# Kernel optimization log

Hardware: AMD Instinct MI355X
Metric: run time of the kernel (lower is better)

The kernel has to match this reference:

```python
import jax, jax.numpy as jnp
import numpy as np

N_NODES = 100000
T = 1024        # number of visits / hyperedges (GRU sequence length)
IN = 128        # in_channel
HID = 256       # hid_channel


def setup_inputs() -> dict:
    key = jax.random.key(0)
    ks = jax.random.split(key, 7)
    X = jax.random.normal(ks[0], (N_NODES, IN), dtype=jnp.float32)
    H = jax.random.uniform(ks[1], (N_NODES, T), dtype=jnp.float32)
    s = 1.0 / np.sqrt(HID)  # torch default GRU init scale
    w_ih = jax.random.uniform(ks[2], (3 * HID, IN), jnp.float32, -s, s)
    w_hh = jax.random.uniform(ks[3], (3 * HID, HID), jnp.float32, -s, s)
    b_ih = jax.random.uniform(ks[4], (3 * HID,), jnp.float32, -s, s)
    b_hh = jax.random.uniform(ks[5], (3 * HID,), jnp.float32, -s, s)
    w_attn = jax.random.uniform(ks[6], (HID,), jnp.float32, -s, s)
    return {"X": X, "H": H, "w_ih": w_ih, "w_hh": w_hh,
            "b_ih": b_ih, "b_hh": b_hh, "w_attn": w_attn}


def _gru(visit_emb, w_ih, w_hh, b_ih, b_hh):
    # Precompute input-side gates for all timesteps: [T, 3H]
    gx = visit_emb @ w_ih.T + b_ih

    def step(h, gx_t):
        gh = h @ w_hh.T + b_hh
        xr, xz, xn = jnp.split(gx_t, 3)
        hr, hz, hn = jnp.split(gh, 3)
        r = jax.nn.sigmoid(xr + hr)
        z = jax.nn.sigmoid(xz + hz)
        n = jnp.tanh(xn + r * hn)
        h_new = (1.0 - z) * n + z * h
        return h_new, h_new

    h0 = jnp.zeros((HID,), visit_emb.dtype)
    _, hs = jax.lax.scan(step, h0, gx)
    return hs  # [T, HID]


def reference(X, H, w_ih, w_hh, b_ih, b_hh, w_attn):
    # visit_emb = H.T @ X : [T, IN]
    visit_emb = H.T @ X
    hs = _gru(visit_emb, w_ih, w_hh, b_ih, b_hh)          # [T, HID]
    alpha = jax.nn.softmax(hs @ w_attn)                    # [T]
    # sum(diag(alpha) @ hs, 0) == alpha-weighted sum of hidden states
    return alpha @ hs                                      # [HID]
```

## Files before the change

kernel.cpp:

```cpp
#include <hip/hip_runtime.h>
#include <hip/hip_fp16.h>

typedef _Float16 half8 __attribute__((ext_vector_type(8)));
typedef float f32x4 __attribute__((ext_vector_type(4)));

#define T_STEPS 1024
#define INC 128
#define HIDC 256
#define G3 768
#define NN 100000
#define KSPLIT 32
#define NCHUNK 3125
#define XS_STRIDE 144

__global__ __launch_bounds__(512) void k_phase1(const float* __restrict__ X,
                                                const float* __restrict__ Hm,
                                                float* __restrict__ part){
  const int tt = blockIdx.x;
  const int ks = blockIdx.y;
  const int t0 = tt * 128;
  const int nbeg = ks * NCHUNK;
  const int nend = nbeg + NCHUNK;
  __shared__ float Hs[16][128];
  __shared__ float Xs[16 * XS_STRIDE];
  const int tid = threadIdx.x;
  const int tx = tid & 15;
  const int ty = tid >> 4;
  const int sr = tid >> 5;
  const int sc = tid & 31;
  const int xskew = tx * 8 + (tx >> 2) * 4;

  float acc[4][8];
  #pragma unroll
  for (int r = 0; r < 4; r++)
    #pragma unroll
    for (int q = 0; q < 8; q++) acc[r][q] = 0.f;

  for (int n0 = nbeg; n0 < nend; n0 += 16){
    int n = n0 + sr;
    float4 hv = {0.f,0.f,0.f,0.f}, xv = {0.f,0.f,0.f,0.f};
    if (n < nend){
      hv = *(const float4*)(Hm + (size_t)n * T_STEPS + t0 + sc * 4);
      xv = *(const float4*)(X  + (size_t)n * INC + sc * 4);
    }
    __syncthreads();
    *(float4*)&Hs[sr][sc * 4] = hv;
    {
      int g = sc >> 1, hf = sc & 1;
      *(float4*)&Xs[sr * XS_STRIDE + g * 8 + (g >> 2) * 4 + hf * 4] = xv;
    }
    __syncthreads();
    #pragma unroll
    for (int i = 0; i < 16; i++){
      float4 h4 = *(const float4*)&Hs[i][ty * 4];
      float4 x0 = *(const float4*)&Xs[i * XS_STRIDE + xskew];
      float4 x1 = *(const float4*)&Xs[i * XS_STRIDE + xskew + 4];
      float xr[8] = {x0.x,x0.y,x0.z,x0.w,x1.x,x1.y,x1.z,x1.w};
      float hr[4] = {h4.x,h4.y,h4.z,h4.w};
      #pragma unroll
      for (int r = 0; r < 4; r++)
        #pragma unroll
        for (int q = 0; q < 8; q++)
          acc[r][q] += hr[r] * xr[q];
    }
  }
  #pragma unroll
  for (int r = 0; r < 4; r++){
    size_t o = ((size_t)ks * T_STEPS + t0 + ty * 4 + r) * INC + tx * 8;
    *(float4*)&part[o]     = make_float4(acc[r][0], acc[r][1], acc[r][2], acc[r][3]);
    *(float4*)&part[o + 4] = make_float4(acc[r][4], acc[r][5], acc[r][6], acc[r][7]);
  }
}

__global__ __launch_bounds__(256) void k_reduce(const float* __restrict__ part,
                                                float* __restrict__ ve){
  int idx = blockIdx.x * 256 + threadIdx.x;
  float s = 0.f;
  #pragma unroll
  for (int ks = 0; ks < KSPLIT; ks++) s += part[(size_t)ks * (T_STEPS * INC) + idx];
  ve[idx] = s;
}

__global__ __launch_bounds__(768) void k_gx(const float* __restrict__ ve,
                                            const float* __restrict__ w_ih,
                                            const float* __restrict__ b_ih,
                                            const float* __restrict__ b_hh,
                                            float* __restrict__ gxq){
  const int t = blockIdx.x;
  const int j = threadIdx.x;
  __shared__ float4 v4[32];
  if (j < 32) v4[j] = *(const float4*)(ve + (size_t)t * INC + j * 4);
  __syncthreads();
  const float4* wr = (const float4*)(w_ih + (size_t)j * INC);
  float a0 = 0.f, a1 = 0.f, a2 = 0.f, a3 = 0.f;
  #pragma unroll
  for (int q = 0; q < 32; q++){
    float4 w = wr[q]; float4 v = v4[q];
    a0 += w.x * v.x; a1 += w.y * v.y; a2 += w.z * v.z; a3 += w.w * v.w;
  }
  float bias = b_ih[j] + (j < 512 ? b_hh[j] : 0.f);
  gxq[(size_t)t * 1024 + (j & 255) * 4 + (j >> 8)] = (a0 + a1) + (a2 + a3) + bias;
}

__global__ __launch_bounds__(1024) void k_gru(const float* __restrict__ w_hh,
                                              const float* __restrict__ b_hh,
                                              const float* __restrict__ gxq,
                                              float* __restrict__ hs){
  const int tid  = threadIdx.x;
  const int w    = tid >> 6;
  const int l    = tid & 63;
  const int col  = l & 15;
  const int quad = l >> 4;
  const int unit = w * 16 + col;

  __shared__ _Float16 hbuf[2][256];

  half8 Bf[3][8];
  #pragma unroll
  for (int g = 0; g < 3; g++){
    const float* wr = w_hh + (size_t)(g * 256 + unit) * HIDC + quad * 8;
    #pragma unroll
    for (int c = 0; c < 8; c++){
      float4 v0 = *(const float4*)(wr + c * 32);
      float4 v1 = *(const float4*)(wr + c * 32 + 4);
      half8 b;
      b[0]=(_Float16)v0.x; b[1]=(_Float16)v0.y; b[2]=(_Float16)v0.z; b[3]=(_Float16)v0.w;
      b[4]=(_Float16)v1.x; b[5]=(_Float16)v1.y; b[6]=(_Float16)v1.z; b[7]=(_Float16)v1.w;
      Bf[g][c] = b;
    }
  }
  const float bn = b_hh[512 + unit];
  float hprev = 0.f;
  if (tid < 256) hbuf[0][tid] = (_Float16)0.f;
  __syncthreads();

  f32x4 gq = *(const f32x4*)(gxq + (size_t)unit * 4);

  for (int t = 0; t < T_STEPS; t++){
    f32x4 dr = {0.f,0.f,0.f,0.f}, dz = {0.f,0.f,0.f,0.f}, dn = {0.f,0.f,0.f,0.f};
    const _Float16* hb = hbuf[t & 1];
    #pragma unroll
    for (int c = 0; c < 8; c++){
      half8 a = *(const half8*)(hb + c * 32 + quad * 8);
      dr = __builtin_amdgcn_mfma_f32_16x16x32_f16(a, Bf[0][c], dr, 0, 0, 0);
      dz = __builtin_amdgcn_mfma_f32_16x16x32_f16(a, Bf[1][c], dz, 0, 0, 0);
      dn = __builtin_amdgcn_mfma_f32_16x16x32_f16(a, Bf[2][c], dn, 0, 0, 0);
    }
    f32x4 gq_n = *(const f32x4*)(gxq + (size_t)(t + 1) * 1024 + unit * 4);

    float r = 1.f / (1.f + __expf(-(gq[0] + dr[0])));
    float z = 1.f / (1.f + __expf(-(gq[1] + dz[0])));
    float pre = gq[2] + r * (dn[0] + bn);
    float ax = fabsf(pre);
    float e = __expf(-2.f * ax);
    float th = (1.f - e) / (1.f + e);
    float n = copysignf(th, pre);
    float hnew = n + z * (hprev - n);
    hprev = hnew;
    if (quad == 0){
      hbuf[(t + 1) & 1][unit] = (_Float16)hnew;
      hs[(size_t)t * HIDC + unit] = hnew;
    }
    gq = gq_n;
    __syncthreads();
  }
}

__global__ __launch_bounds__(64) void k_logits(const float* __restrict__ hs,
                                               const float* __restrict__ w_attn,
                                               float* __restrict__ logits){
  int t = blockIdx.x;
  int l = threadIdx.x;
  float4 hv = *(const float4*)(hs + (size_t)t * HIDC + l * 4);
  float4 wv = *(const float4*)(w_attn + l * 4);
  float p = hv.x * wv.x + hv.y * wv.y + hv.z * wv.z + hv.w * wv.w;
  #pragma unroll
  for (int o = 32; o > 0; o >>= 1) p += __shfl_down(p, o);
  if (l == 0) logits[t] = p;
}

__global__ __launch_bounds__(1024) void k_attn(const float* __restrict__ logits,
                                               const float* __restrict__ hs,
                                               float* __restrict__ out){
  __shared__ float sm[1024];
  __shared__ float al[1024];
  __shared__ float ps[4][HIDC];
  int tid = threadIdx.x;
  float lg = logits[tid];
  sm[tid] = lg; __syncthreads();
  for (int s = 512; s > 0; s >>= 1){
    if (tid < s) sm[tid] = fmaxf(sm[tid], sm[tid + s]);
    __syncthreads();
  }
  float mx = sm[0]; __syncthreads();
  float e = __expf(lg - mx);
  sm[tid] = e; __syncthreads();
  for (int s = 512; s > 0; s >>= 1){
    if (tid < s) sm[tid] += sm[tid + s];
    __syncthreads();
  }
  float inv = 1.f / sm[0];
  al[tid] = e * inv;
  __syncthreads();
  int c = tid & 255; int tq = tid >> 8;
  float acc = 0.f;
  for (int t = tq; t < T_STEPS; t += 4) acc += al[t] * hs[(size_t)t * HIDC + c];
  ps[tq][c] = acc; __syncthreads();
  if (tid < HIDC) out[tid] = (ps[0][tid] + ps[1][tid]) + (ps[2][tid] + ps[3][tid]);
}

extern "C" void kernel_launch(void* const* d_in, const int* in_sizes, int n_in,
                              void* d_out, int out_size, void* d_ws, size_t ws_size,
                              hipStream_t stream){
  const float* X      = (const float*)d_in[0];
  const float* Hm     = (const float*)d_in[1];
  const float* w_ih   = (const float*)d_in[2];
  const float* w_hh   = (const float*)d_in[3];
  const float* b_ih   = (const float*)d_in[4];
  const float* b_hh   = (const float*)d_in[5];
  const float* w_attn = (const float*)d_in[6];
  float* out = (float*)d_out;

  float* ws     = (float*)d_ws;
  float* part   = ws;
  float* ve     = part + 4194304;
  float* gxq    = ve + 131072;
  float* hs     = gxq + 1049600;
  float* logits = hs + 262144;

  k_phase1<<<dim3(8, 32), 512, 0, stream>>>(X, Hm, part);
  k_reduce<<<512, 256, 0, stream>>>(part, ve);
  k_gx<<<1024, 768, 0, stream>>>(ve, w_ih, b_ih, b_hh, gxq);
  k_gru<<<1, 1024, 0, stream>>>(w_hh, b_hh, gxq, hs);
  k_logits<<<1024, 64, 0, stream>>>(hs, w_attn, logits);
  k_attn<<<1, 1024, 0, stream>>>(logits, hs, out);
}
```

Before: 2.317 ms.

## Prefetch next tile in phase1, remap blocks to XCDs, use lightweight barriers

The phase1 H^T·X kernel now issues the global loads for the next 16-row tile before computing on the current tile in shared memory. This overlaps memory latency with the FMA work. Block indices are remapped so that the blocks sharing an XCD work on neighbouring K-split chunks, which may improve L2 locality. Both phase1 and the GRU loop swap __syncthreads for a raw s_barrier plus an LDS-only waitcnt, so the barrier no longer waits on outstanding global loads and stores. This relies on correct manual waitcnt handling.

```diff
diff --git a/kernel.cpp b/kernel.cpp
--- a/kernel.cpp
+++ b/kernel.cpp
@@ -16,8 +16,11 @@
 __global__ __launch_bounds__(512) void k_phase1(const float* __restrict__ X,
                                                 const float* __restrict__ Hm,
                                                 float* __restrict__ part){
-  const int tt = blockIdx.x;
-  const int ks = blockIdx.y;
+  const int bid = blockIdx.x;
+  const int xcd = bid & 7;
+  const int idx = bid >> 3;
+  const int ks  = xcd * 4 + (idx & 3);
+  const int tt  = idx >> 2;
   const int t0 = tt * 128;
   const int nbeg = ks * NCHUNK;
   const int nend = nbeg + NCHUNK;
@@ -36,20 +39,37 @@
     #pragma unroll
     for (int q = 0; q < 8; q++) acc[r][q] = 0.f;
 
-  for (int n0 = nbeg; n0 < nend; n0 += 16){
-    int n = n0 + sr;
-    float4 hv = {0.f,0.f,0.f,0.f}, xv = {0.f,0.f,0.f,0.f};
+  float4 hv = make_float4(0.f,0.f,0.f,0.f), xv = make_float4(0.f,0.f,0.f,0.f);
+  {
+    int n = nbeg + sr;
     if (n < nend){
       hv = *(const float4*)(Hm + (size_t)n * T_STEPS + t0 + sc * 4);
       xv = *(const float4*)(X  + (size_t)n * INC + sc * 4);
     }
-    __syncthreads();
+  }
+
+  for (int n0 = nbeg; n0 < nend; n0 += 16){
+    __builtin_amdgcn_s_barrier();
+    asm volatile("" ::: "memory");
     *(float4*)&Hs[sr][sc * 4] = hv;
     {
       int g = sc >> 1, hf = sc & 1;
       *(float4*)&Xs[sr * XS_STRIDE + g * 8 + (g >> 2) * 4 + hf * 4] = xv;
     }
-    __syncthreads();
+    asm volatile("s_waitcnt lgkmcnt(0)" ::: "memory");
+    __builtin_amdgcn_s_barrier();
+    asm volatile("" ::: "memory");
+
+    {
+      int nn = n0 + 16 + sr;
+      hv = make_float4(0.f,0.f,0.f,0.f);
+      xv = make_float4(0.f,0.f,0.f,0.f);
+      if (nn < nend){
+        hv = *(const float4*)(Hm + (size_t)nn * T_STEPS + t0 + sc * 4);
+        xv = *(const float4*)(X  + (size_t)nn * INC + sc * 4);
+      }
+    }
+
     #pragma unroll
     for (int i = 0; i < 16; i++){
       float4 h4 = *(const float4*)&Hs[i][ty * 4];
@@ -161,8 +181,10 @@
       hbuf[(t + 1) & 1][unit] = (_Float16)hnew;
       hs[(size_t)t * HIDC + unit] = hnew;
     }
+    asm volatile("s_waitcnt lgkmcnt(0)" ::: "memory");
+    __builtin_amdgcn_s_barrier();
+    asm volatile("" ::: "memory");
     gq = gq_n;
-    __syncthreads();
   }
 }
 
@@ -228,7 +250,7 @@
   float* hs     = gxq + 1049600;
   float* logits = hs + 262144;
 
-  k_phase1<<<dim3(8, 32), 512, 0, stream>>>(X, Hm, part);
+  k_phase1<<<256, 512, 0, stream>>>(X, Hm, part);
   k_reduce<<<512, 256, 0, stream>>>(part, ve);
   k_gx<<<1024, 768, 0, stream>>>(ve, w_ih, b_ih, b_hh, gxq);
   k_gru<<<1, 1024, 0, stream>>>(w_hh, b_hh, gxq, hs);
```

Measured after the change: 2.317 ms. No clear change (-0.0%).
